# Performance work log

Hardware: AMD Instinct MI355X
Metric: run time of the kernel (lower is better)

Reference implementation:

```python
import jax, jax.numpy as jnp
import numpy as np
import math

B, S_IN, S_OUT, D_IN, D_OUT, G = 8, 1024, 1024, 96, 96, 8
LN_EPS = 1e-5


def setup_inputs() -> dict:
    key = jax.random.key(0)
    k_x, k_m, k_p, k_l = jax.random.split(key, 4)
    x = jax.random.normal(k_x, (B, S_IN, D_IN), dtype=jnp.float32)
    M = jax.random.uniform(k_m, (D_OUT, D_IN), minval=-0.5, maxval=0.5, dtype=jnp.float32)
    P = jax.random.uniform(k_p, (D_OUT, D_OUT, G), minval=-0.1, maxval=0.1, dtype=jnp.float32)
    Linker = jax.random.uniform(k_l, (S_IN, S_OUT), minval=-0.1, maxval=0.1, dtype=jnp.float32)
    gamma = jnp.ones((D_OUT,), dtype=jnp.float32)
    beta = jnp.zeros((D_OUT,), dtype=jnp.float32)
    return {"x": x, "M": M, "P": P, "Linker": Linker, "gamma": gamma, "beta": beta}


def _layer_norm(z, gamma, beta):
    mu = jnp.mean(z, axis=-1, keepdims=True)
    var = jnp.mean(jnp.square(z - mu), axis=-1, keepdims=True)
    return (z - mu) * jax.lax.rsqrt(var + LN_EPS) * gamma + beta


def reference(x, M, P, Linker, gamma, beta):
    # Z = x @ M^T, then LayerNorm over feature dim
    Z0 = jnp.einsum('bsj,ij->bsi', x, M)           # (B, S_in, D_out)
    Z = _layer_norm(Z0, gamma, beta)
    # periods[i,j,g] = i*(D_out*G) + j*G + g + 2
    periods = (jnp.arange(D_OUT * D_OUT * G, dtype=jnp.float32)
               .reshape(D_OUT, D_OUT, G) + 2.0)
    k = jnp.arange(S_IN, dtype=jnp.float32)
    # phi[s,i,j,g] = cos(2*pi*s / periods[i,j,g])
    phi = jnp.cos((2.0 * math.pi) * k[:, None, None, None] / periods[None])
    # fuse basis reduction: W[s,i,j] = sum_g P[i,j,g] * phi[s,i,j,g]
    W = jnp.einsum('sijg,ijg->sij', phi, P)        # (S_in, D_out, D_out)
    # T[b,s,i] = sum_j Z[b,s,j] * W[s,i,j]
    T = jnp.einsum('bsj,sij->bsi', Z, W)           # (B, S_in, D_out)
    # sequence transform via Linker
    U = jnp.einsum('bsi,st->bti', T, Linker)       # (B, S_out, D_out)
    # shared residual: x @ M^T (pre-LN) through the same Linker
    residual = jnp.einsum('bsi,st->bti', Z0, Linker)
    return U + residual
```

## Files before the change

### kernel.cpp

```cpp
#include <hip/hip_runtime.h>
#include <cstdint>
#include <cstddef>

#define BSTRIDE 98304

typedef __attribute__((ext_vector_type(8))) short short8;
typedef __attribute__((ext_vector_type(4))) float f32x4;

__device__ __forceinline__ uint16_t f2bf(float x) {
    uint32_t u = __float_as_uint(x);
    return (uint16_t)((u + 0x7FFF + ((u >> 16) & 1)) >> 16);
}
__device__ __forceinline__ float bf2f(uint16_t b) {
    return __uint_as_float(((uint32_t)b) << 16);
}

struct SmemS {
    union { float xs[8][96]; float zr[96][8]; } u;
    float zs[96][8];
    float part[4][8][96];
    uint16_t W[96][100];
    float ps1[8][12], ps2[8][12], stats[8][2];
};
union SmemF { SmemS f; struct { float T[64][65]; } kl; };

__global__ __launch_bounds__(384, 5) void k_fused(
    const float* __restrict__ x, const float* __restrict__ M,
    const float* __restrict__ P, const float* __restrict__ L,
    const float* __restrict__ gamma, const float* __restrict__ beta,
    uint16_t* __restrict__ Lt, uint16_t* __restrict__ Vt)
{
    __shared__ SmemF sm;
    const int t  = threadIdx.x;
    const int bx = blockIdx.x;

    if (bx >= 1024) {
        const int bx2 = bx - 1024;
        const int s0 = (bx2 & 15) * 64, t0 = (bx2 >> 4) * 64;
        if (t < 64) {
            for (int r = 0; r < 64; ++r)
                sm.kl.T[r][t] = L[(size_t)(s0 + r) * 1024 + t0 + t];
        }
        __syncthreads();
        if (t < 64) {
            uint16_t* orow = Lt + (size_t)(t0 + t) * 1024 + s0;
            #pragma unroll
            for (int c4 = 0; c4 < 16; ++c4) {
                uint32_t u01 = (uint32_t)f2bf(sm.kl.T[c4*4+0][t]) |
                               ((uint32_t)f2bf(sm.kl.T[c4*4+1][t]) << 16);
                uint32_t u23 = (uint32_t)f2bf(sm.kl.T[c4*4+2][t]) |
                               ((uint32_t)f2bf(sm.kl.T[c4*4+3][t]) << 16);
                uint2 o; o.x = u01; o.y = u23;
                *(uint2*)(orow + c4 * 4) = o;
            }
        }
        return;
    }

    const int s = bx;
    const int e = t % 96;
    const int q = t / 96;
    const int jq = q * 24;

    {
        float* xf = &sm.f.u.xs[0][0];
        #pragma unroll
        for (int r = 0; r < 2; ++r) {
            int idx = t + r * 384;
            int b = idx / 96, j = idx - b * 96;
            xf[idx] = x[(size_t)b * BSTRIDE + (size_t)s * 96 + j];
        }
    }
    __syncthreads();

    {
        float acc[8] = {0.f,0.f,0.f,0.f,0.f,0.f,0.f,0.f};
        const float* Mp = M + (size_t)e * 96 + jq;
        #pragma unroll
        for (int jj4 = 0; jj4 < 6; ++jj4) {
            float4 m4 = *(const float4*)(Mp + jj4 * 4);
            #pragma unroll
            for (int b = 0; b < 8; ++b) {
                float4 xv = *(const float4*)&sm.f.u.xs[b][jq + jj4 * 4];
                acc[b] = fmaf(m4.x, xv.x,
                         fmaf(m4.y, xv.y,
                         fmaf(m4.z, xv.z,
                         fmaf(m4.w, xv.w, acc[b]))));
            }
        }
        #pragma unroll
        for (int b = 0; b < 8; ++b) sm.f.part[q][b][e] = acc[b];
    }
    __syncthreads();

    {
        #pragma unroll
        for (int bb = 0; bb < 2; ++bb) {
            int b = q * 2 + bb;
            float v = sm.f.part[0][b][e] + sm.f.part[1][b][e] +
                      sm.f.part[2][b][e] + sm.f.part[3][b][e];
            sm.f.u.zr[e][b] = v;
        }
    }
    __syncthreads();

    if (t < 96) {
        const int b = t / 12, grp = t % 12;
        float s1 = 0.f, s2 = 0.f;
        #pragma unroll
        for (int k = 0; k < 8; ++k) {
            float v = sm.f.u.zr[grp * 8 + k][b];
            s1 += v; s2 += v * v;
        }
        sm.f.ps1[b][grp] = s1; sm.f.ps2[b][grp] = s2;
    }
    __syncthreads();
    if (t < 8) {
        float s1 = 0.f, s2 = 0.f;
        #pragma unroll
        for (int k = 0; k < 12; ++k) { s1 += sm.f.ps1[t][k]; s2 += sm.f.ps2[t][k]; }
        float mu  = s1 * (1.f / 96.f);
        float var = s2 * (1.f / 96.f) - mu * mu;
        sm.f.stats[t][0] = mu;
        sm.f.stats[t][1] = rsqrtf(var + 1e-5f);
    }
    __syncthreads();

    {
        float gm = gamma[e], bt = beta[e];
        #pragma unroll
        for (int bb = 0; bb < 2; ++bb) {
            int b = q * 2 + bb;
            sm.f.zs[e][b] =
                (sm.f.u.zr[e][b] - sm.f.stats[b][0]) * sm.f.stats[b][1] * gm + bt;
        }
    }

    {
        const float sf = (float)s;
        const int j = e;
        #pragma unroll 1
        for (int ii = 0; ii < 24; ii += 2) {
            const int i0 = q * 24 + ii;
            const float* Pp = P + ((size_t)i0 * 96 + j) * 8;
            float4 pa = *(const float4*)(Pp);
            float4 pb = *(const float4*)(Pp + 4);
            float4 pc = *(const float4*)(Pp + 768);
            float4 pd = *(const float4*)(Pp + 772);
            float pv0[8] = {pa.x, pa.y, pa.z, pa.w, pb.x, pb.y, pb.z, pb.w};
            float pv1[8] = {pc.x, pc.y, pc.z, pc.w, pd.x, pd.y, pd.z, pd.w};
            float base0 = (float)((i0 * 96 + j) * 8 + 2);
            float base1 = base0 + 768.0f;
            float w0 = 0.f, w1 = 0.f;
            #pragma unroll
            for (int g = 0; g < 8; ++g) {
                float inv0 = __builtin_amdgcn_rcpf(base0 + (float)g);
                float inv1 = __builtin_amdgcn_rcpf(base1 + (float)g);
                float a0 = sf * inv0; a0 -= floorf(a0);
                float a1 = sf * inv1; a1 -= floorf(a1);
                w0 = fmaf(pv0[g], __builtin_amdgcn_cosf(a0), w0);
                w1 = fmaf(pv1[g], __builtin_amdgcn_cosf(a1), w1);
            }
            *(uint32_t*)&sm.f.W[j][i0] =
                (uint32_t)f2bf(w0) | ((uint32_t)f2bf(w1) << 16);
        }
    }
    __syncthreads();

    {
        float tacc[8] = {0.f,0.f,0.f,0.f,0.f,0.f,0.f,0.f};
        #pragma unroll 4
        for (int jj = 0; jj < 24; ++jj) {
            int j = jq + jj;
            float w = bf2f(sm.f.W[j][e]);
            float4 z0 = *(const float4*)&sm.f.zs[j][0];
            float4 z1 = *(const float4*)&sm.f.zs[j][4];
            tacc[0] = fmaf(z0.x, w, tacc[0]);
            tacc[1] = fmaf(z0.y, w, tacc[1]);
            tacc[2] = fmaf(z0.z, w, tacc[2]);
            tacc[3] = fmaf(z0.w, w, tacc[3]);
            tacc[4] = fmaf(z1.x, w, tacc[4]);
            tacc[5] = fmaf(z1.y, w, tacc[5]);
            tacc[6] = fmaf(z1.z, w, tacc[6]);
            tacc[7] = fmaf(z1.w, w, tacc[7]);
        }
        #pragma unroll
        for (int b = 0; b < 8; ++b) sm.f.part[q][b][e] = tacc[b];
    }
    __syncthreads();

    {
        #pragma unroll
        for (int bb = 0; bb < 2; ++bb) {
            int b = q * 2 + bb;
            float T = sm.f.part[0][b][e] + sm.f.part[1][b][e] +
                      sm.f.part[2][b][e] + sm.f.part[3][b][e];
            float z0 = sm.f.u.zr[e][b];
            Vt[((size_t)b * 96 + e) * 1024 + s] = f2bf(T + z0);
        }
    }
}

__global__ __launch_bounds__(256) void k3_mfma(
    const uint16_t* __restrict__ Lt, const uint16_t* __restrict__ Vt,
    float* __restrict__ out)
{
    __shared__ float racc[3][64][25];
    const int lane = threadIdx.x & 63;
    const int kw   = threadIdx.x >> 6;
    const int m    = lane & 15;
    const int quad = lane >> 4;
    const int t0   = blockIdx.x * 16;
    const int b    = blockIdx.y;

    const uint16_t* Lp = Lt + (size_t)(t0 + m) * 1024 + kw * 256 + quad * 8;
    const uint16_t* Vp = Vt + ((size_t)b * 96 + m) * 1024 + kw * 256 + quad * 8;

    f32x4 acc[6];
    #pragma unroll
    for (int ii = 0; ii < 6; ++ii) acc[ii] = (f32x4){0.f, 0.f, 0.f, 0.f};

    short8 a = *(const short8*)Lp;
    short8 bv[6];
    #pragma unroll
    for (int ii = 0; ii < 6; ++ii)
        bv[ii] = *(const short8*)(Vp + (size_t)ii * 16 * 1024);

    for (int kc = 0; kc < 7; ++kc) {
        short8 an = *(const short8*)(Lp + (kc + 1) * 32);
        short8 bn[6];
        #pragma unroll
        for (int ii = 0; ii < 6; ++ii)
            bn[ii] = *(const short8*)(Vp + (size_t)ii * 16 * 1024 + (kc + 1) * 32);
        #pragma unroll
        for (int ii = 0; ii < 6; ++ii)
            acc[ii] = __builtin_amdgcn_mfma_f32_16x16x32_bf16(a, bv[ii], acc[ii], 0, 0, 0);
        a = an;
        #pragma unroll
        for (int ii = 0; ii < 6; ++ii) bv[ii] = bn[ii];
    }
    #pragma unroll
    for (int ii = 0; ii < 6; ++ii)
        acc[ii] = __builtin_amdgcn_mfma_f32_16x16x32_bf16(a, bv[ii], acc[ii], 0, 0, 0);

    if (kw > 0) {
        #pragma unroll
        for (int ii = 0; ii < 6; ++ii)
            #pragma unroll
            for (int r = 0; r < 4; ++r)
                racc[kw - 1][lane][ii * 4 + r] = acc[ii][r];
    }
    __syncthreads();
    if (kw == 0) {
        float* po = out + (size_t)b * BSTRIDE;
        #pragma unroll
        for (int ii = 0; ii < 6; ++ii)
            #pragma unroll
            for (int r = 0; r < 4; ++r)
                po[(size_t)(t0 + quad * 4 + r) * 96 + ii * 16 + m] =
                    acc[ii][r] + racc[0][lane][ii * 4 + r] +
                    racc[1][lane][ii * 4 + r] + racc[2][lane][ii * 4 + r];
    }
}

extern "C" void kernel_launch(void* const* d_in, const int* in_sizes, int n_in,
                              void* d_out, int out_size, void* d_ws, size_t ws_size,
                              hipStream_t stream)
{
    const float* x     = (const float*)d_in[0];
    const float* M     = (const float*)d_in[1];
    const float* P     = (const float*)d_in[2];
    const float* Lnk   = (const float*)d_in[3];
    const float* gamma = (const float*)d_in[4];
    const float* beta  = (const float*)d_in[5];
    float* out = (float*)d_out;

    uint8_t* ws = (uint8_t*)d_ws;
    uint16_t* Lt = (uint16_t*)ws;
    uint16_t* Vt = (uint16_t*)(ws + 2097152);

    k_fused <<<1280, 384, 0, stream>>>(x, M, P, Lnk, gamma, beta, Lt, Vt);
    k3_mfma <<<dim3(64, 8), 256, 0, stream>>>(Lt, Vt, out);
}
```

Baseline: 124.6 us.

## Alias W with partials in LDS, raise occupancy, split GEMM K across eight waves

In the fused kernel, the W tile and the partial-sum buffer now share shared memory through a union, which shrinks the LDS footprint. The min-blocks hint rises from 5 to 7, and the W loop uses strength-reduced pointers, hardware fract and unroll 2. The final Linker GEMM now uses 512 threads, with each of 8 waves covering a 128-wide K slice. Each wave loads its whole slice up front and the slices are reduced across all waves through shared memory. This trades deeper per-wave pipelining and extra register pressure for more parallelism, and adds an extra barrier in the fused kernel.

```diff
diff --git a/kernel.cpp b/kernel.cpp
--- a/kernel.cpp
+++ b/kernel.cpp
@@ -18,13 +18,12 @@
 struct SmemS {
     union { float xs[8][96]; float zr[96][8]; } u;
     float zs[96][8];
-    float part[4][8][96];
-    uint16_t W[96][100];
+    union { uint16_t W[96][100]; float part[4][8][96]; } w;
     float ps1[8][12], ps2[8][12], stats[8][2];
 };
 union SmemF { SmemS f; struct { float T[64][65]; } kl; };
 
-__global__ __launch_bounds__(384, 5) void k_fused(
+__global__ __launch_bounds__(384, 7) void k_fused(
     const float* __restrict__ x, const float* __restrict__ M,
     const float* __restrict__ P, const float* __restrict__ L,
     const float* __restrict__ gamma, const float* __restrict__ beta,
@@ -89,7 +88,7 @@
             }
         }
         #pragma unroll
-        for (int b = 0; b < 8; ++b) sm.f.part[q][b][e] = acc[b];
+        for (int b = 0; b < 8; ++b) sm.f.w.part[q][b][e] = acc[b];
     }
     __syncthreads();
 
@@ -97,8 +96,8 @@
         #pragma unroll
         for (int bb = 0; bb < 2; ++bb) {
             int b = q * 2 + bb;
-            float v = sm.f.part[0][b][e] + sm.f.part[1][b][e] +
-                      sm.f.part[2][b][e] + sm.f.part[3][b][e];
+            float v = sm.f.w.part[0][b][e] + sm.f.w.part[1][b][e] +
+                      sm.f.w.part[2][b][e] + sm.f.w.part[3][b][e];
             sm.f.u.zr[e][b] = v;
         }
     }
@@ -139,40 +138,40 @@
     {
         const float sf = (float)s;
         const int j = e;
-        #pragma unroll 1
+        const float* Pp = P + ((size_t)jq * 96 + j) * 8;
+        float base0 = (float)((jq * 96 + j) * 8 + 2);
+        uint16_t* wrow = &sm.f.w.W[j][jq];
+        #pragma unroll 2
         for (int ii = 0; ii < 24; ii += 2) {
-            const int i0 = q * 24 + ii;
-            const float* Pp = P + ((size_t)i0 * 96 + j) * 8;
             float4 pa = *(const float4*)(Pp);
             float4 pb = *(const float4*)(Pp + 4);
             float4 pc = *(const float4*)(Pp + 768);
             float4 pd = *(const float4*)(Pp + 772);
             float pv0[8] = {pa.x, pa.y, pa.z, pa.w, pb.x, pb.y, pb.z, pb.w};
             float pv1[8] = {pc.x, pc.y, pc.z, pc.w, pd.x, pd.y, pd.z, pd.w};
-            float base0 = (float)((i0 * 96 + j) * 8 + 2);
-            float base1 = base0 + 768.0f;
             float w0 = 0.f, w1 = 0.f;
             #pragma unroll
             for (int g = 0; g < 8; ++g) {
                 float inv0 = __builtin_amdgcn_rcpf(base0 + (float)g);
-                float inv1 = __builtin_amdgcn_rcpf(base1 + (float)g);
-                float a0 = sf * inv0; a0 -= floorf(a0);
-                float a1 = sf * inv1; a1 -= floorf(a1);
+                float inv1 = __builtin_amdgcn_rcpf(base0 + (float)(768 + g));
+                float a0 = __builtin_amdgcn_fractf(sf * inv0);
+                float a1 = __builtin_amdgcn_fractf(sf * inv1);
                 w0 = fmaf(pv0[g], __builtin_amdgcn_cosf(a0), w0);
                 w1 = fmaf(pv1[g], __builtin_amdgcn_cosf(a1), w1);
             }
-            *(uint32_t*)&sm.f.W[j][i0] =
+            *(uint32_t*)(wrow + ii) =
                 (uint32_t)f2bf(w0) | ((uint32_t)f2bf(w1) << 16);
-        }
-    }
-    __syncthreads();
-
-    {
-        float tacc[8] = {0.f,0.f,0.f,0.f,0.f,0.f,0.f,0.f};
+            Pp += 1536; base0 += 1536.0f;
+        }
+    }
+    __syncthreads();
+
+    float tacc[8] = {0.f,0.f,0.f,0.f,0.f,0.f,0.f,0.f};
+    {
         #pragma unroll 4
         for (int jj = 0; jj < 24; ++jj) {
             int j = jq + jj;
-            float w = bf2f(sm.f.W[j][e]);
+            float w = bf2f(sm.f.w.W[j][e]);
             float4 z0 = *(const float4*)&sm.f.zs[j][0];
             float4 z1 = *(const float4*)&sm.f.zs[j][4];
             tacc[0] = fmaf(z0.x, w, tacc[0]);
@@ -184,8 +183,11 @@
             tacc[6] = fmaf(z1.z, w, tacc[6]);
             tacc[7] = fmaf(z1.w, w, tacc[7]);
         }
-        #pragma unroll
-        for (int b = 0; b < 8; ++b) sm.f.part[q][b][e] = tacc[b];
+    }
+    __syncthreads();
+    {
+        #pragma unroll
+        for (int b = 0; b < 8; ++b) sm.f.w.part[q][b][e] = tacc[b];
     }
     __syncthreads();
 
@@ -193,19 +195,19 @@
         #pragma unroll
         for (int bb = 0; bb < 2; ++bb) {
             int b = q * 2 + bb;
-            float T = sm.f.part[0][b][e] + sm.f.part[1][b][e] +
-                      sm.f.part[2][b][e] + sm.f.part[3][b][e];
+            float T = sm.f.w.part[0][b][e] + sm.f.w.part[1][b][e] +
+                      sm.f.w.part[2][b][e] + sm.f.w.part[3][b][e];
             float z0 = sm.f.u.zr[e][b];
             Vt[((size_t)b * 96 + e) * 1024 + s] = f2bf(T + z0);
         }
     }
 }
 
-__global__ __launch_bounds__(256) void k3_mfma(
+__global__ __launch_bounds__(512, 2) void k3_mfma(
     const uint16_t* __restrict__ Lt, const uint16_t* __restrict__ Vt,
     float* __restrict__ out)
 {
-    __shared__ float racc[3][64][25];
+    __shared__ float racc[8][64][25];
     const int lane = threadIdx.x & 63;
     const int kw   = threadIdx.x >> 6;
     const int m    = lane & 15;
@@ -213,53 +215,44 @@
     const int t0   = blockIdx.x * 16;
     const int b    = blockIdx.y;
 
-    const uint16_t* Lp = Lt + (size_t)(t0 + m) * 1024 + kw * 256 + quad * 8;
-    const uint16_t* Vp = Vt + ((size_t)b * 96 + m) * 1024 + kw * 256 + quad * 8;
+    const uint16_t* Lp = Lt + (size_t)(t0 + m) * 1024 + kw * 128 + quad * 8;
+    const uint16_t* Vp = Vt + ((size_t)b * 96 + m) * 1024 + kw * 128 + quad * 8;
+
+    short8 a[4];
+    short8 bv[4][6];
+    #pragma unroll
+    for (int kc = 0; kc < 4; ++kc) {
+        a[kc] = *(const short8*)(Lp + kc * 32);
+        #pragma unroll
+        for (int ii = 0; ii < 6; ++ii)
+            bv[kc][ii] = *(const short8*)(Vp + (size_t)ii * 16 * 1024 + kc * 32);
+    }
 
     f32x4 acc[6];
     #pragma unroll
     for (int ii = 0; ii < 6; ++ii) acc[ii] = (f32x4){0.f, 0.f, 0.f, 0.f};
-
-    short8 a = *(const short8*)Lp;
-    short8 bv[6];
+    #pragma unroll
+    for (int kc = 0; kc < 4; ++kc)
+        #pragma unroll
+        for (int ii = 0; ii < 6; ++ii)
+            acc[ii] = __builtin_amdgcn_mfma_f32_16x16x32_bf16(a[kc], bv[kc][ii], acc[ii], 0, 0, 0);
+
     #pragma unroll
     for (int ii = 0; ii < 6; ++ii)
-        bv[ii] = *(const short8*)(Vp + (size_t)ii * 16 * 1024);
-
-    for (int kc = 0; kc < 7; ++kc) {
-        short8 an = *(const short8*)(Lp + (kc + 1) * 32);
-        short8 bn[6];
-        #pragma unroll
-        for (int ii = 0; ii < 6; ++ii)
-            bn[ii] = *(const short8*)(Vp + (size_t)ii * 16 * 1024 + (kc + 1) * 32);
-        #pragma unroll
-        for (int ii = 0; ii < 6; ++ii)
-            acc[ii] = __builtin_amdgcn_mfma_f32_16x16x32_bf16(a, bv[ii], acc[ii], 0, 0, 0);
-        a = an;
-        #pragma unroll
-        for (int ii = 0; ii < 6; ++ii) bv[ii] = bn[ii];
-    }
-    #pragma unroll
-    for (int ii = 0; ii < 6; ++ii)
-        acc[ii] = __builtin_amdgcn_mfma_f32_16x16x32_bf16(a, bv[ii], acc[ii], 0, 0, 0);
-
-    if (kw > 0) {
-        #pragma unroll
-        for (int ii = 0; ii < 6; ++ii)
-            #pragma unroll
-            for (int r = 0; r < 4; ++r)
-                racc[kw - 1][lane][ii * 4 + r] = acc[ii][r];
-    }
-    __syncthreads();
-    if (kw == 0) {
-        float* po = out + (size_t)b * BSTRIDE;
-        #pragma unroll
-        for (int ii = 0; ii < 6; ++ii)
-            #pragma unroll
-            for (int r = 0; r < 4; ++r)
-                po[(size_t)(t0 + quad * 4 + r) * 96 + ii * 16 + m] =
-                    acc[ii][r] + racc[0][lane][ii * 4 + r] +
-                    racc[1][lane][ii * 4 + r] + racc[2][lane][ii * 4 + r];
+        #pragma unroll
+        for (int r = 0; r < 4; ++r)
+            racc[kw][lane][ii * 4 + r] = acc[ii][r];
+    __syncthreads();
+
+    float* po = out + (size_t)b * BSTRIDE;
+    #pragma unroll
+    for (int sl = 0; sl < 3; ++sl) {
+        int slot = kw * 3 + sl;
+        int ii = slot >> 2, r = slot & 3;
+        float v = 0.f;
+        #pragma unroll
+        for (int k = 0; k < 8; ++k) v += racc[k][lane][slot];
+        po[(size_t)(t0 + quad * 4 + r) * 96 + ii * 16 + m] = v;
     }
 }
 
@@ -280,5 +273,5 @@
     uint16_t* Vt = (uint16_t*)(ws + 2097152);
 
     k_fused <<<1280, 384, 0, stream>>>(x, M, P, Lnk, gamma, beta, Lt, Vt);
-    k3_mfma <<<dim3(64, 8), 256, 0, stream>>>(Lt, Vt, out);
-}
+    k3_mfma <<<dim3(64, 8), 512, 0, stream>>>(Lt, Vt, out);
+}
```

After: 115.5 us. 1.08x faster.
